# Kernel tuning notes

Measured on AMD Instinct MI355X. Metric: run time of the kernel, lower is better.

Reference implementation:

```python
import jax, jax.numpy as jnp
import numpy as np

WS = 7            # window_size
HEADS = 3
HEAD_DIM = 32
DISP = WS // 2    # displacement = 3
SCALE = HEAD_DIM ** -0.5
NEG = float('-inf')

def _create_mask(upper_lower, left_right):
    m = np.zeros((WS * WS, WS * WS), dtype=np.float32)
    if upper_lower:
        m[-DISP * WS:, :-DISP * WS] = NEG
        m[:-DISP * WS, -DISP * WS:] = NEG
    if left_right:
        m = m.reshape(WS, WS, WS, WS)
        m[:, -DISP:, :, :-DISP] = NEG
        m[:, :-DISP, :, -DISP:] = NEG
        m = m.reshape(WS * WS, WS * WS)
    return m

_UL = jnp.asarray(_create_mask(True, False))   # upper/lower boundary mask [49,49]
_LR = jnp.asarray(_create_mask(False, True))   # left/right boundary mask  [49,49]
_idx = np.array([[i, j] for i in range(WS) for j in range(WS)])
_REL = _idx[None, :, :] - _idx[:, None, :] + WS - 1  # static relative indices [49,49,2]


def setup_inputs() -> dict:
    key = jax.random.key(0)
    ks = jax.random.split(key, 10)
    dim = 96
    inner = HEADS * HEAD_DIM  # 96
    mid = dim                 # dim // 16 = 6 < 10 -> middle_channel = dim per CA code
    B, H, W = 8, 224, 224
    s = lambda k, shape: jax.random.normal(k, shape, jnp.float32) * 0.02
    return {
        "x": jax.random.normal(ks[0], (B, H, W, dim), jnp.float32),
        "w_qkv": s(ks[1], (dim, inner * 3)),
        "pos_emb": jax.random.normal(ks[2], (2 * WS - 1, 2 * WS - 1), jnp.float32),
        "w_out": s(ks[3], (inner, dim)),
        "b_out": jnp.zeros((dim,), jnp.float32),
        "mlp1_w1": s(ks[4], (dim, mid)), "mlp1_b1": jnp.zeros((mid,), jnp.float32),
        "mlp1_w2": s(ks[5], (mid, dim)), "mlp1_b2": jnp.zeros((dim,), jnp.float32),
        "mlp2_w1": s(ks[6], (dim, mid)), "mlp2_b1": jnp.zeros((mid,), jnp.float32),
        "mlp2_w2": s(ks[7], (mid, dim)), "mlp2_b2": jnp.zeros((dim,), jnp.float32),
    }


def reference(x, w_qkv, pos_emb, w_out, b_out,
              mlp1_w1, mlp1_b1, mlp1_w2, mlp1_b2,
              mlp2_w1, mlp2_b1, mlp2_w2, mlp2_b2):
    B, H, W, C = x.shape
    nw_h, nw_w = H // WS, W // WS
    # cyclic shift
    xs = jnp.roll(x, (-DISP, -DISP), axis=(1, 2))
    # qkv projection (no bias)
    q, k, v = jnp.split(xs @ w_qkv, 3, axis=-1)

    def to_win(t):  # [B,H,W,inner] -> [B,heads,n_windows,49,head_dim]
        t = t.reshape(B, nw_h, WS, nw_w, WS, HEADS, HEAD_DIM)
        return t.transpose(0, 5, 1, 3, 2, 4, 6).reshape(B, HEADS, nw_h * nw_w, WS * WS, HEAD_DIM)

    q, k, v = to_win(q), to_win(k), to_win(v)
    dots = jnp.einsum('bhwid,bhwjd->bhwij', q, k) * SCALE
    dots = dots + pos_emb[_REL[..., 0], _REL[..., 1]]  # relative position bias [49,49]
    # boundary window masks for shifted attention
    dots = dots.at[:, :, -nw_w:].add(_UL)
    dots = dots.at[:, :, nw_w - 1::nw_w].add(_LR)
    attn = jax.nn.softmax(dots, axis=-1)
    out = jnp.einsum('bhwij,bhwjd->bhwid', attn, v)
    out = out.reshape(B, HEADS, nw_h, nw_w, WS, WS, HEAD_DIM)
    out = out.transpose(0, 2, 4, 3, 5, 1, 6).reshape(B, H, W, HEADS * HEAD_DIM)
    out = out @ w_out + b_out
    out = jnp.roll(out, (DISP, DISP), axis=(1, 2))  # cyclic back-shift
    # CA channel attention: avg/max pool over spatial -> two MLPs -> sigmoid gate
    avg = out.mean(axis=(1, 2))                     # [B,C]
    mx = out.max(axis=(1, 2))                       # [B,C]
    a = jax.nn.relu(avg @ mlp1_w1 + mlp1_b1) @ mlp1_w2 + mlp1_b2
    m = jax.nn.relu(mx @ mlp2_w1 + mlp2_b1) @ mlp2_w2 + mlp2_b2
    gate = jax.nn.sigmoid(a + m)
    return out * gate[:, None, None, :]
```

## Files before the change

kernel.cpp:

```cpp
#include <hip/hip_runtime.h>
#include <hip/hip_bf16.h>

typedef __attribute__((ext_vector_type(8))) __bf16 bf16x8;
typedef __attribute__((ext_vector_type(4))) float f32x4;
typedef unsigned short u16;
typedef unsigned long long u64;

#define SCALE2   (0.17677669529663687f * 1.44269504088896f)
#define LOG2E    1.44269504088896f

static __device__ __forceinline__ u16 f2b(float f) {
    union { __bf16 h; u16 u; } z; z.h = (__bf16)f; return z.u;
}
static __device__ __forceinline__ float bu2f(u16 s) {
    union { unsigned u; float f; } z; z.u = ((unsigned)s) << 16; return z.f;
}
static __device__ __forceinline__ f32x4 mfma16(bf16x8 a, bf16x8 b, f32x4 c) {
    return __builtin_amdgcn_mfma_f32_16x16x32_bf16(a, b, c, 0, 0, 0);
}
static __device__ __forceinline__ bf16x8 ldfrag(const u16* p) {
    return *(const bf16x8*)p;
}
static __device__ __forceinline__ u64 pack4(float a, float b, float c, float d) {
    union { __bf16 h[4]; u64 q; } z;
    z.h[0] = (__bf16)a; z.h[1] = (__bf16)b; z.h[2] = (__bf16)c; z.h[3] = (__bf16)d;
    return z.q;
}
static __device__ __forceinline__ bf16x8 pack8(float4 a, float4 b) {
    union { __bf16 h[8]; bf16x8 v; } z;
    z.h[0] = (__bf16)a.x; z.h[1] = (__bf16)a.y; z.h[2] = (__bf16)a.z; z.h[3] = (__bf16)a.w;
    z.h[4] = (__bf16)b.x; z.h[5] = (__bf16)b.y; z.h[6] = (__bf16)b.z; z.h[7] = (__bf16)b.w;
    return z.v;
}
static __device__ __forceinline__ void st4(u16* base, int row, int col, u64 v) {
    *(u64*)&base[(row << 6) + (col ^ ((row & 7) << 3))] = v;
}
static __device__ __forceinline__ bf16x8 ld8(const u16* base, int row, int col) {
    return *(const bf16x8*)&base[(row << 6) + (col ^ ((row & 7) << 3))];
}

__global__ __launch_bounds__(256) void prep_weights(
    const float* __restrict__ w_qkv, const float* __restrict__ w_out,
    u16* __restrict__ wsq, u16* __restrict__ wso)
{
    int idx = blockIdx.x * 256 + threadIdx.x;
    if (idx < 27648) {
        int e = idx & 7, lA = (idx >> 3) & 63;
        int rest = idx >> 9;
        int ks = rest % 3, sec = (rest / 3) % 6, h = rest / 18;
        int krow = ks * 32 + (lA >> 4) * 8 + e;
        int n = lA & 15;
        int gcol;
        if (sec < 2)      gcol = h * 32 + sec * 16 + n;
        else if (sec < 4) gcol = 96 + h * 32 + (sec - 2) * 16 + n;
        else              gcol = 192 + h * 32 + (sec - 4) * 16 + n;
        wsq[idx] = f2b(w_qkv[krow * 288 + gcol]);
    }
    if (idx < 9216) {
        int e = idx & 7, lA = (idx >> 3) & 63;
        int rest = idx >> 9;
        int nt = rest % 6, h = rest / 6;
        int krow = h * 32 + (lA >> 4) * 8 + e;
        wso[idx] = f2b(w_out[krow * 96 + nt * 16 + (lA & 15)]);
    }
}

__global__ __launch_bounds__(256) void prep_bias(
    const float* __restrict__ pos_emb, float* __restrict__ biasT)
{
    int idx = blockIdx.x * 256 + threadIdx.x;
    if (idx >= 16384) return;
    int j = idx & 63, i = (idx >> 6) & 63, t = idx >> 12;
    float v;
    if (j >= 49) v = -1e30f;
    else if (i >= 49) v = 0.f;
    else {
        int ir = i / 7, ic = i - ir * 7, jr = j / 7, jc = j - jr * 7;
        v = pos_emb[(jr - ir + 6) * 13 + (jc - ic + 6)] * LOG2E;
        if ((t & 1) && ((ir >= 4) != (jr >= 4))) v = -1e30f;
        if ((t & 2) && ((ic >= 4) != (jc >= 4))) v = -1e30f;
    }
    biasT[idx] = v;
}

__global__ __launch_bounds__(256, 4) void swin_attn_mfma(
    const float* __restrict__ x,
    const float* __restrict__ biasT,
    const u16*  __restrict__ wsq,
    const u16*  __restrict__ wso,
    const float* __restrict__ b_out,
    float* __restrict__ outf,
    u16*  __restrict__ outw,
    float* __restrict__ psum_win,
    float* __restrict__ pmax_win,
    int write_bf16)
{
    __shared__ __attribute__((aligned(16))) u16 qk_s[64 * 64];
    __shared__ __attribute__((aligned(16))) u16 vT_s[32 * 64];
    __shared__ __attribute__((aligned(16))) u16 p_s[64 * 64];

    const int blk = blockIdx.x;
    const int b = blk >> 10, win = blk & 1023;
    const int wh = win >> 5, ww = win & 31;
    const int tid = threadIdx.x;
    const int w = tid >> 6, l = tid & 63, lr = l & 15, lg = l >> 4;
    const int myrow = 16 * w + lr;

    bf16x8 ax0, ax1, ax2;
    {
        int sr = wh * 7 + myrow / 7 + 3;  if (sr >= 224) sr -= 224;
        int sc = ww * 7 + myrow % 7 + 3;  if (sc >= 224) sc -= 224;
        const float* xr = x + (((size_t)b * 224 + sr) * 224 + sc) * 96 + lg * 8;
        ax0 = pack8(*(const float4*)(xr +  0), *(const float4*)(xr +  4));
        ax1 = pack8(*(const float4*)(xr + 32), *(const float4*)(xr + 36));
        ax2 = pack8(*(const float4*)(xr + 64), *(const float4*)(xr + 68));
    }

    const float* bt = biasT + (((wh == 31) ? 1 : 0) + ((ww == 31) ? 2 : 0)) * 4096
                    + myrow * 64 + lg * 4;
    const float4 bias0 = *(const float4*)(bt);
    const float4 bias1 = *(const float4*)(bt + 16);
    const float4 bias2 = *(const float4*)(bt + 32);
    const float4 bias3 = *(const float4*)(bt + 48);

    const u16* wsq_l = wsq + l * 8;
    const u16* wso_l = wso + l * 8;

    f32x4 proj[6];
    #pragma unroll
    for (int nt = 0; nt < 6; ++nt) proj[nt] = (f32x4){0.f, 0.f, 0.f, 0.f};

    u64 kq0, kq1, vt0, vt1;

    auto GEMM1 = [&](int h) {
        #pragma unroll
        for (int sec = 0; sec < 6; ++sec) {
            const u16* wb = wsq_l + (size_t)(h * 18 + sec * 3) * 512;
            f32x4 c = {0.f, 0.f, 0.f, 0.f};
            if (sec < 4) {
                c = mfma16(ldfrag(wb), ax0, c);
                c = mfma16(ldfrag(wb + 512), ax1, c);
                c = mfma16(ldfrag(wb + 1024), ax2, c);
                u64 pk = pack4(c[0], c[1], c[2], c[3]);
                if (sec == 0)      st4(qk_s, myrow,      lg * 4, pk);
                else if (sec == 1) st4(qk_s, myrow, 16 + lg * 4, pk);
                else if (sec == 2) kq0 = pk;
                else               kq1 = pk;
            } else {
                c = mfma16(ax0, ldfrag(wb), c);
                c = mfma16(ax1, ldfrag(wb + 512), c);
                c = mfma16(ax2, ldfrag(wb + 1024), c);
                u64 pk = pack4(c[0], c[1], c[2], c[3]);
                if (sec == 4) vt0 = pk; else vt1 = pk;
            }
        }
    };
    auto FLUSH_KV = [&]() {
        st4(qk_s, myrow, 32 + lg * 4, kq0);
        st4(qk_s, myrow, 48 + lg * 4, kq1);
        st4(vT_s, lr,      16 * w + lg * 4, vt0);
        st4(vT_s, 16 + lr, 16 * w + lg * 4, vt1);
    };

    GEMM1(0);
    FLUSH_KV();
    __syncthreads();

    #pragma unroll
    for (int h = 0; h < 3; ++h) {
        bf16x8 bq = ld8(qk_s, myrow, lg * 8);

        if (h < 2) GEMM1(h + 1);

        f32x4 S[4];
        #pragma unroll
        for (int jt = 0; jt < 4; ++jt) {
            f32x4 z = {0.f, 0.f, 0.f, 0.f};
            S[jt] = mfma16(ld8(qk_s, jt * 16 + lr, 32 + lg * 8), bq, z);
        }

        float ssum = 0.f;
        float e0[4], e1[4], e2[4], e3[4];
        #pragma unroll
        for (int reg = 0; reg < 4; ++reg) {
            e0[reg] = exp2f(fmaf(S[0][reg], SCALE2, bias0[reg])); ssum += e0[reg];
            e1[reg] = exp2f(fmaf(S[1][reg], SCALE2, bias1[reg])); ssum += e1[reg];
            e2[reg] = exp2f(fmaf(S[2][reg], SCALE2, bias2[reg])); ssum += e2[reg];
            e3[reg] = exp2f(fmaf(S[3][reg], SCALE2, bias3[reg])); ssum += e3[reg];
        }
        ssum += __shfl_xor(ssum, 16);
        ssum += __shfl_xor(ssum, 32);
        float inv = 1.f / ssum;
        st4(p_s, myrow,      lg * 4, pack4(e0[0], e0[1], e0[2], e0[3]));
        st4(p_s, myrow, 16 + lg * 4, pack4(e1[0], e1[1], e1[2], e1[3]));
        st4(p_s, myrow, 32 + lg * 4, pack4(e2[0], e2[1], e2[2], e2[3]));
        st4(p_s, myrow, 48 + lg * 4, pack4(e3[0], e3[1], e3[2], e3[3]));

        bf16x8 bp0 = ld8(p_s, myrow, lg * 8);
        bf16x8 bp1 = ld8(p_s, myrow, 32 + lg * 8);
        #pragma unroll
        for (int mt = 0; mt < 2; ++mt) {
            f32x4 c = {0.f, 0.f, 0.f, 0.f};
            c = mfma16(ld8(vT_s, mt * 16 + lr,  0 + lg * 8), bp0, c);
            c = mfma16(ld8(vT_s, mt * 16 + lr, 32 + lg * 8), bp1, c);
            st4(p_s, myrow, mt * 16 + lg * 4,
                pack4(c[0] * inv, c[1] * inv, c[2] * inv, c[3] * inv));
        }

        bf16x8 ao = ld8(p_s, myrow, lg * 8);
        #pragma unroll
        for (int nt = 0; nt < 6; ++nt)
            proj[nt] = mfma16(ao, ldfrag(wso_l + (size_t)(h * 6 + nt) * 512),
                              proj[nt]);

        __syncthreads();
        if (h < 2) {
            FLUSH_KV();
            __syncthreads();
        }
    }

    float bo[6];
    #pragma unroll
    for (int nt = 0; nt < 6; ++nt) bo[nt] = b_out[nt * 16 + lr];
    float csum[6], cmax[6];
    #pragma unroll
    for (int nt = 0; nt < 6; ++nt) { csum[nt] = 0.f; cmax[nt] = -1e30f; }
    const int tok0 = 16 * w + lg * 4;
    const int r0t = tok0 / 7, c0t = tok0 - r0t * 7;
    #pragma unroll
    for (int reg = 0; reg < 4; ++reg) {
        if (tok0 + reg < 49) {
            int rr = r0t, cc = c0t + reg;
            if (cc >= 7) { cc -= 7; rr += 1; }
            int sr = wh * 7 + rr + 3;  if (sr >= 224) sr -= 224;
            int sc = ww * 7 + cc + 3;  if (sc >= 224) sc -= 224;
            size_t o0 = (((size_t)b * 224 + sr) * 224 + sc) * 96 + lr;
            #pragma unroll
            for (int nt = 0; nt < 6; ++nt) {
                float v = proj[nt][reg] + bo[nt];
                if (write_bf16) outw[o0 + nt * 16] = f2b(v);
                else            outf[o0 + nt * 16] = v;
                csum[nt] += v;
                cmax[nt] = fmaxf(cmax[nt], v);
            }
        }
    }
    #pragma unroll
    for (int nt = 0; nt < 6; ++nt) {
        csum[nt] += __shfl_xor(csum[nt], 16);
        csum[nt] += __shfl_xor(csum[nt], 32);
        cmax[nt] = fmaxf(cmax[nt], __shfl_xor(cmax[nt], 16));
        cmax[nt] = fmaxf(cmax[nt], __shfl_xor(cmax[nt], 32));
    }
    float* rsum = (float*)p_s;
    float* rmax = rsum + 384;
    __syncthreads();
    if (lg == 0) {
        #pragma unroll
        for (int nt = 0; nt < 6; ++nt) {
            rsum[w * 96 + nt * 16 + lr] = csum[nt];
            rmax[w * 96 + nt * 16 + lr] = cmax[nt];
        }
    }
    __syncthreads();
    if (tid < 96) {
        size_t o = ((size_t)b * 1024 + win) * 96 + tid;
        psum_win[o] = rsum[tid] + rsum[96 + tid] + rsum[192 + tid] + rsum[288 + tid];
        pmax_win[o] = fmaxf(fmaxf(rmax[tid], rmax[96 + tid]),
                            fmaxf(rmax[192 + tid], rmax[288 + tid]));
    }
}

__global__ __launch_bounds__(384) void gate_kernel(
    const float* __restrict__ psum, const float* __restrict__ pmax,
    const float* __restrict__ w11, const float* __restrict__ b11,
    const float* __restrict__ w12, const float* __restrict__ b12,
    const float* __restrict__ w21, const float* __restrict__ b21,
    const float* __restrict__ w22, const float* __restrict__ b22,
    float* __restrict__ gate)
{
    const int b = blockIdx.x;
    const int tid = threadIdx.x;
    const int c = tid % 96, sub = tid / 96;
    __shared__ float ls[384], lm[384];
    __shared__ float avg[96], mx[96], h1[96], h2[96];

    float s = 0.f, m = -1e30f;
    for (int k = sub * 256; k < sub * 256 + 256; ++k) {
        size_t o = ((size_t)b * 1024 + k) * 96 + c;
        s += psum[o];
        m = fmaxf(m, pmax[o]);
    }
    ls[tid] = s; lm[tid] = m;
    __syncthreads();
    if (tid < 96) {
        s = ls[c] + ls[96 + c] + ls[192 + c] + ls[288 + c];
        m = fmaxf(fmaxf(lm[c], lm[96 + c]), fmaxf(lm[192 + c], lm[288 + c]));
        avg[c] = s * (1.0f / 50176.0f);
        mx[c]  = m;
    }
    __syncthreads();
    if (tid < 96) {
        float sa = b11[c], sm = b21[c];
        for (int ic = 0; ic < 96; ++ic) {
            sa = fmaf(avg[ic], w11[ic * 96 + c], sa);
            sm = fmaf(mx[ic],  w21[ic * 96 + c], sm);
        }
        h1[c] = fmaxf(sa, 0.f);
        h2[c] = fmaxf(sm, 0.f);
    }
    __syncthreads();
    if (tid < 96) {
        float a = b12[c], m2 = b22[c];
        for (int hh = 0; hh < 96; ++hh) {
            a  = fmaf(h1[hh], w12[hh * 96 + c], a);
            m2 = fmaf(h2[hh], w22[hh * 96 + c], m2);
        }
        float g = a + m2;
        gate[b * 96 + c] = 1.0f / (1.0f + __expf(-g));
    }
}

__global__ __launch_bounds__(256) void scale_bf16_kernel(
    const u16* __restrict__ outw, float* __restrict__ out,
    const float* __restrict__ gate)
{
    const size_t total8 = 38535168u / 8;
    for (size_t i8 = (size_t)blockIdx.x * blockDim.x + threadIdx.x; i8 < total8;
         i8 += (size_t)gridDim.x * blockDim.x) {
        size_t base = i8 * 8;
        int c = (int)(base % 96);
        int b = (int)(base / ((size_t)50176 * 96));
        u64 pk0 = *(const u64*)(outw + base);
        u64 pk1 = *(const u64*)(outw + base + 4);
        float4 g0 = *(const float4*)(gate + b * 96 + c);
        float4 g1 = *(const float4*)(gate + b * 96 + c + 4);
        float4 o0, o1;
        o0.x = bu2f((u16)(pk0      )) * g0.x;
        o0.y = bu2f((u16)(pk0 >> 16)) * g0.y;
        o0.z = bu2f((u16)(pk0 >> 32)) * g0.z;
        o0.w = bu2f((u16)(pk0 >> 48)) * g0.w;
        o1.x = bu2f((u16)(pk1      )) * g1.x;
        o1.y = bu2f((u16)(pk1 >> 16)) * g1.y;
        o1.z = bu2f((u16)(pk1 >> 32)) * g1.z;
        o1.w = bu2f((u16)(pk1 >> 48)) * g1.w;
        *(float4*)(out + base)     = o0;
        *(float4*)(out + base + 4) = o1;
    }
}

__global__ __launch_bounds__(256) void scale_f32_kernel(
    float* __restrict__ out, const float* __restrict__ gate)
{
    const size_t total4 = 38535168u / 4;
    for (size_t i4 = (size_t)blockIdx.x * blockDim.x + threadIdx.x; i4 < total4;
         i4 += (size_t)gridDim.x * blockDim.x) {
        size_t base = i4 * 4;
        int c = (int)(base % 96);
        int b = (int)(base / ((size_t)50176 * 96));
        float4 u = ((const float4*)out)[i4];
        float4 g = *(const float4*)(gate + b * 96 + c);
        float4 o;
        o.x = u.x * g.x; o.y = u.y * g.y; o.z = u.z * g.z; o.w = u.w * g.w;
        ((float4*)out)[i4] = o;
    }
}

extern "C" void kernel_launch(void* const* d_in, const int* in_sizes, int n_in,
                              void* d_out, int out_size, void* d_ws, size_t ws_size,
                              hipStream_t stream) {
    const float* x     = (const float*)d_in[0];
    const float* wqkv  = (const float*)d_in[1];
    const float* pos   = (const float*)d_in[2];
    const float* wout  = (const float*)d_in[3];
    const float* bout  = (const float*)d_in[4];
    const float* m1w1  = (const float*)d_in[5];
    const float* m1b1  = (const float*)d_in[6];
    const float* m1w2  = (const float*)d_in[7];
    const float* m1b2  = (const float*)d_in[8];
    const float* m2w1  = (const float*)d_in[9];
    const float* m2b1  = (const float*)d_in[10];
    const float* m2w2  = (const float*)d_in[11];
    const float* m2b2  = (const float*)d_in[12];
    float* out = (float*)d_out;

    float* psum_win = (float*)d_ws;
    float* pmax_win = psum_win + 8 * 1024 * 96;
    float* gatep    = pmax_win + 8 * 1024 * 96;
    u16*   wsq      = (u16*)(gatep + 8 * 96);
    u16*   wso      = wsq + 27648;
    float* biasT    = (float*)(wso + 9216);
    u16*   outw     = (u16*)(biasT + 16384);

    const size_t base_bytes = (size_t)((char*)outw - (char*)d_ws);
    const size_t outw_bytes = (size_t)8 * 50176 * 96 * sizeof(u16);
    const int use_bf16 = (ws_size >= base_bytes + outw_bytes) ? 1 : 0;

    hipLaunchKernelGGL(prep_weights, dim3(108), dim3(256), 0, stream,
                       wqkv, wout, wsq, wso);
    hipLaunchKernelGGL(prep_bias, dim3(64), dim3(256), 0, stream,
                       pos, biasT);
    hipLaunchKernelGGL(swin_attn_mfma, dim3(8192), dim3(256), 0, stream,
                       x, biasT, wsq, wso, bout,
                       use_bf16 ? nullptr : out, use_bf16 ? outw : nullptr,
                       psum_win, pmax_win, use_bf16);
    hipLaunchKernelGGL(gate_kernel, dim3(8), dim3(384), 0, stream,
                       psum_win, pmax_win, m1w1, m1b1, m1w2, m1b2,
                       m2w1, m2b1, m2w2, m2b2, gatep);
    if (use_bf16) {
        hipLaunchKernelGGL(scale_bf16_kernel, dim3(2048), dim3(256), 0, stream,
                           outw, out, gatep);
    } else {
        hipLaunchKernelGGL(scale_f32_kernel, dim3(2048), dim3(256), 0, stream,
                           out, gatep);
    }
}
```

Measured before the change: 273.0 us.

## Double-buffer per-head QK/V in LDS and drop extra barrier per head

Q/K and V^T LDS buffers are duplicated so the next head's QKV projection writes straight into the alternate buffer, instead of holding K/V in registers and flushing them after a barrier. This removes one __syncthreads and the flush step per head, and reuses the current Q/K buffer for the attention output instead of p_s. The bias table is also rearranged into the per-lane MFMA fragment order so each lane reads 64 contiguous bytes. LDS use grows by about 12 KB per block, which may reduce occupancy under the 4-blocks-per-CU launch bound.

```diff
diff --git a/kernel.cpp b/kernel.cpp
--- a/kernel.cpp
+++ b/kernel.cpp
@@ -70,7 +70,10 @@
 {
     int idx = blockIdx.x * 256 + threadIdx.x;
     if (idx >= 16384) return;
-    int j = idx & 63, i = (idx >> 6) & 63, t = idx >> 12;
+    int reg = idx & 3, jt = (idx >> 2) & 3, l = (idx >> 4) & 63;
+    int w = (idx >> 10) & 3, t = idx >> 12;
+    int i = 16 * w + (l & 15);
+    int j = jt * 16 + (l >> 4) * 4 + reg;
     float v;
     if (j >= 49) v = -1e30f;
     else if (i >= 49) v = 0.f;
@@ -95,8 +98,10 @@
     float* __restrict__ pmax_win,
     int write_bf16)
 {
-    __shared__ __attribute__((aligned(16))) u16 qk_s[64 * 64];
-    __shared__ __attribute__((aligned(16))) u16 vT_s[32 * 64];
+    __shared__ __attribute__((aligned(16))) u16 qk0_s[64 * 64];
+    __shared__ __attribute__((aligned(16))) u16 qk1_s[64 * 64];
+    __shared__ __attribute__((aligned(16))) u16 vT0_s[32 * 64];
+    __shared__ __attribute__((aligned(16))) u16 vT1_s[32 * 64];
     __shared__ __attribute__((aligned(16))) u16 p_s[64 * 64];
 
     const int blk = blockIdx.x;
@@ -105,6 +110,13 @@
     const int tid = threadIdx.x;
     const int w = tid >> 6, l = tid & 63, lr = l & 15, lg = l >> 4;
     const int myrow = 16 * w + lr;
+
+    const int wtype = ((wh == 31) ? 1 : 0) + ((ww == 31) ? 2 : 0);
+    const float4* btp = (const float4*)(biasT + (((size_t)wtype * 4 + w) * 64 + l) * 16);
+    const float4 bias0 = btp[0];
+    const float4 bias1 = btp[1];
+    const float4 bias2 = btp[2];
+    const float4 bias3 = btp[3];
 
     bf16x8 ax0, ax1, ax2;
     {
@@ -116,13 +128,6 @@
         ax2 = pack8(*(const float4*)(xr + 64), *(const float4*)(xr + 68));
     }
 
-    const float* bt = biasT + (((wh == 31) ? 1 : 0) + ((ww == 31) ? 2 : 0)) * 4096
-                    + myrow * 64 + lg * 4;
-    const float4 bias0 = *(const float4*)(bt);
-    const float4 bias1 = *(const float4*)(bt + 16);
-    const float4 bias2 = *(const float4*)(bt + 32);
-    const float4 bias3 = *(const float4*)(bt + 48);
-
     const u16* wsq_l = wsq + l * 8;
     const u16* wso_l = wso + l * 8;
 
@@ -130,9 +135,7 @@
     #pragma unroll
     for (int nt = 0; nt < 6; ++nt) proj[nt] = (f32x4){0.f, 0.f, 0.f, 0.f};
 
-    u64 kq0, kq1, vt0, vt1;
-
-    auto GEMM1 = [&](int h) {
+    auto GEMM1 = [&](int h, u16* qkb, u16* vtb) {
         #pragma unroll
         for (int sec = 0; sec < 6; ++sec) {
             const u16* wb = wsq_l + (size_t)(h * 18 + sec * 3) * 512;
@@ -141,42 +144,34 @@
                 c = mfma16(ldfrag(wb), ax0, c);
                 c = mfma16(ldfrag(wb + 512), ax1, c);
                 c = mfma16(ldfrag(wb + 1024), ax2, c);
-                u64 pk = pack4(c[0], c[1], c[2], c[3]);
-                if (sec == 0)      st4(qk_s, myrow,      lg * 4, pk);
-                else if (sec == 1) st4(qk_s, myrow, 16 + lg * 4, pk);
-                else if (sec == 2) kq0 = pk;
-                else               kq1 = pk;
+                st4(qkb, myrow, (sec < 2 ? 0 : 32) + (sec & 1) * 16 + lg * 4,
+                    pack4(c[0], c[1], c[2], c[3]));
             } else {
                 c = mfma16(ax0, ldfrag(wb), c);
                 c = mfma16(ax1, ldfrag(wb + 512), c);
                 c = mfma16(ax2, ldfrag(wb + 1024), c);
-                u64 pk = pack4(c[0], c[1], c[2], c[3]);
-                if (sec == 4) vt0 = pk; else vt1 = pk;
+                st4(vtb, (sec - 4) * 16 + lr, 16 * w + lg * 4,
+                    pack4(c[0], c[1], c[2], c[3]));
             }
         }
     };
-    auto FLUSH_KV = [&]() {
-        st4(qk_s, myrow, 32 + lg * 4, kq0);
-        st4(qk_s, myrow, 48 + lg * 4, kq1);
-        st4(vT_s, lr,      16 * w + lg * 4, vt0);
-        st4(vT_s, 16 + lr, 16 * w + lg * 4, vt1);
-    };
-
-    GEMM1(0);
-    FLUSH_KV();
+
+    GEMM1(0, qk0_s, vT0_s);
     __syncthreads();
 
     #pragma unroll
     for (int h = 0; h < 3; ++h) {
-        bf16x8 bq = ld8(qk_s, myrow, lg * 8);
-
-        if (h < 2) GEMM1(h + 1);
-
+        u16* qkb = (h & 1) ? qk1_s : qk0_s;
+        u16* vtb = (h & 1) ? vT1_s : vT0_s;
+
+        if (h < 2) GEMM1(h + 1, (h & 1) ? qk0_s : qk1_s, (h & 1) ? vT0_s : vT1_s);
+
+        bf16x8 bq = ld8(qkb, myrow, lg * 8);
         f32x4 S[4];
         #pragma unroll
         for (int jt = 0; jt < 4; ++jt) {
             f32x4 z = {0.f, 0.f, 0.f, 0.f};
-            S[jt] = mfma16(ld8(qk_s, jt * 16 + lr, 32 + lg * 8), bq, z);
+            S[jt] = mfma16(ld8(qkb, jt * 16 + lr, 32 + lg * 8), bq, z);
         }
 
         float ssum = 0.f;
@@ -201,23 +196,19 @@
         #pragma unroll
         for (int mt = 0; mt < 2; ++mt) {
             f32x4 c = {0.f, 0.f, 0.f, 0.f};
-            c = mfma16(ld8(vT_s, mt * 16 + lr,  0 + lg * 8), bp0, c);
-            c = mfma16(ld8(vT_s, mt * 16 + lr, 32 + lg * 8), bp1, c);
-            st4(p_s, myrow, mt * 16 + lg * 4,
+            c = mfma16(ld8(vtb, mt * 16 + lr,  0 + lg * 8), bp0, c);
+            c = mfma16(ld8(vtb, mt * 16 + lr, 32 + lg * 8), bp1, c);
+            st4(qkb, myrow, mt * 16 + lg * 4,
                 pack4(c[0] * inv, c[1] * inv, c[2] * inv, c[3] * inv));
         }
 
-        bf16x8 ao = ld8(p_s, myrow, lg * 8);
+        bf16x8 ao = ld8(qkb, myrow, lg * 8);
         #pragma unroll
         for (int nt = 0; nt < 6; ++nt)
             proj[nt] = mfma16(ao, ldfrag(wso_l + (size_t)(h * 6 + nt) * 512),
                               proj[nt]);
 
-        __syncthreads();
-        if (h < 2) {
-            FLUSH_KV();
-            __syncthreads();
-        }
+        if (h < 2) __syncthreads();
     }
 
     float bo[6];
```

Result: faster. 227.6 us (-16.7%).
